# Kernel optimization log

Measured on AMD Instinct MI355X. Metric: run time of the kernel, lower is better.

The kernel has to match this reference:

```python
import jax, jax.numpy as jnp
import numpy as np

B = 256
H, W = 8, 16          # input_resolution for channels=256
C = 768               # dim = channels*3
WS = 4                # window_size
SHIFT = 2             # shift_size
NH = 12               # num_heads
HD = C // NH          # head_dim = 64
HID = 1024            # mlp hidden = channels*4
N = WS * WS           # tokens per window = 16
NW = (H // WS) * (W // WS)  # windows per image = 8
LN_EPS = 1e-5


def _rel_pos_index():
    coords = np.stack(np.meshgrid(np.arange(WS), np.arange(WS), indexing='ij'))  # [2,ws,ws]
    cf = coords.reshape(2, -1)                      # [2, N]
    rel = (cf[:, :, None] - cf[:, None, :]).transpose(1, 2, 0)  # [N, N, 2]
    rel[:, :, 0] += WS - 1
    rel[:, :, 1] += WS - 1
    rel[:, :, 0] *= 2 * WS - 1
    return jnp.asarray(rel.sum(-1))                 # [N, N] int


def _attn_mask():
    img = np.zeros((H, W))
    slices = (slice(0, -WS), slice(-WS, -SHIFT), slice(-SHIFT, None))
    cnt = 0
    for hs in slices:
        for ws_ in slices:
            img[hs, ws_] = cnt
            cnt += 1
    mw = img.reshape(H // WS, WS, W // WS, WS).transpose(0, 2, 1, 3).reshape(-1, N)  # [nW, N]
    am = mw[:, None, :] - mw[:, :, None]            # [nW, N, N]
    return jnp.asarray(np.where(am != 0, -100.0, 0.0).astype(np.float32))


REL_IDX = _rel_pos_index()
ATTN_MASK = _attn_mask()


def _ln(x, g, b):
    m = x.mean(-1, keepdims=True)
    v = ((x - m) ** 2).mean(-1, keepdims=True)
    return (x - m) / jnp.sqrt(v + LN_EPS) * g + b


def setup_inputs() -> dict:
    key = jax.random.key(0)
    ks = jax.random.split(key, 8)
    s = 0.02
    return {
        'x': jax.random.normal(ks[0], (B, H * W, C), jnp.float32),
        'ln1_g': jnp.ones((C,), jnp.float32),
        'ln1_b': jnp.zeros((C,), jnp.float32),
        'qkv_w': jax.random.normal(ks[1], (C, 3 * C), jnp.float32) * s,
        'qkv_b': jnp.zeros((3 * C,), jnp.float32),
        'proj_w': jax.random.normal(ks[2], (C, C), jnp.float32) * s,
        'proj_b': jnp.zeros((C,), jnp.float32),
        'rel_table': jax.random.normal(ks[3], ((2 * WS - 1) * (2 * WS - 1), NH), jnp.float32) * s,
        'ln2_g': jnp.ones((C,), jnp.float32),
        'ln2_b': jnp.zeros((C,), jnp.float32),
        'fc1_w': jax.random.normal(ks[4], (C, HID), jnp.float32) * s,
        'fc1_b': jax.random.normal(ks[5], (HID,), jnp.float32) * 1e-6,
        'fc2_w': jax.random.normal(ks[6], (HID, C), jnp.float32) * s,
        'fc2_b': jax.random.normal(ks[7], (C,), jnp.float32) * 1e-6,
    }


def reference(x, ln1_g, ln1_b, qkv_w, qkv_b, proj_w, proj_b, rel_table,
              ln2_g, ln2_b, fc1_w, fc1_b, fc2_w, fc2_b):
    # --- norm1 + cyclic shift + window partition ---
    h = _ln(x, ln1_g, ln1_b).reshape(B, H, W, C)
    h = jnp.roll(h, (-SHIFT, -SHIFT), axis=(1, 2))
    hw = h.reshape(B, H // WS, WS, W // WS, WS, C).transpose(0, 1, 3, 2, 4, 5)
    hw = hw.reshape(B * NW, N, C)                   # (num_windows*B, N, C)
    # --- window attention with relative position bias + shift mask ---
    qkv = (hw @ qkv_w + qkv_b).reshape(B * NW, N, 3, NH, HD).transpose(2, 0, 3, 1, 4)
    q, k, v = qkv[0] * (HD ** -0.5), qkv[1], qkv[2]  # [Bn, NH, N, HD]
    attn = jnp.einsum('bhnd,bhmd->bhnm', q, k)      # [Bn, NH, N, N]
    bias = rel_table[REL_IDX].transpose(2, 0, 1)    # [NH, N, N]
    attn = attn + bias[None]
    attn = attn.reshape(B, NW, NH, N, N) + ATTN_MASK[None, :, None]
    attn = jax.nn.softmax(attn.reshape(B * NW, NH, N, N), axis=-1)
    o = jnp.einsum('bhnm,bhmd->bhnd', attn, v).transpose(0, 2, 1, 3).reshape(B * NW, N, C)
    o = o @ proj_w + proj_b
    # --- window reverse + reverse shift + residual ---
    o = o.reshape(B, H // WS, W // WS, WS, WS, C).transpose(0, 1, 3, 2, 4, 5).reshape(B, H, W, C)
    o = jnp.roll(o, (SHIFT, SHIFT), axis=(1, 2)).reshape(B, H * W, C)
    x = x + o
    # --- MLP block (dropout is identity at inference) ---
    y = _ln(x, ln2_g, ln2_b)
    y = jax.nn.gelu(y @ fc1_w + fc1_b, approximate=False)
    return x + (y @ fc2_w + fc2_b)
```

## Files before the change

### kernel.cpp

```cpp
#include <hip/hip_runtime.h>
#include <stdint.h>
#include <stddef.h>

typedef __attribute__((ext_vector_type(8))) short bf16x8;
typedef __attribute__((ext_vector_type(4))) float f32x4;
typedef __attribute__((ext_vector_type(4))) unsigned int uint4v;

static __device__ __forceinline__ unsigned short f2bf(float f) {
  unsigned int u = __builtin_bit_cast(unsigned int, f);
  unsigned int r = (u + 0x7FFFu + ((u >> 16) & 1u)) >> 16;
  return (unsigned short)r;
}
static __device__ __forceinline__ float bf2f(unsigned short h) {
  unsigned int u = ((unsigned int)h) << 16;
  return __builtin_bit_cast(float, u);
}
static __device__ __forceinline__ unsigned int pk2(float a, float b) {
  return (unsigned int)f2bf(a) | ((unsigned int)f2bf(b) << 16);
}

static __device__ __forceinline__ void gld16(const void* g, void* l) {
  __builtin_amdgcn_global_load_lds(
      (const __attribute__((address_space(1))) void*)g,
      (__attribute__((address_space(3))) void*)l, 16, 0, 0);
}

__global__ void transpose_cast_all(const float* __restrict__ s0, unsigned short* __restrict__ d0,
                                   const float* __restrict__ s1, unsigned short* __restrict__ d1,
                                   const float* __restrict__ s2, unsigned short* __restrict__ d2,
                                   const float* __restrict__ s3, unsigned short* __restrict__ d3) {
  __shared__ float tile[32][33];
  const int b = blockIdx.x;
  const float* src; unsigned short* dst; int R, C, nbx, bi;
  if (b < 1728)      { src = s0; dst = d0; R = 768;  C = 2304; nbx = 72; bi = b; }
  else if (b < 2304) { src = s1; dst = d1; R = 768;  C = 768;  nbx = 24; bi = b - 1728; }
  else if (b < 3072) { src = s2; dst = d2; R = 768;  C = 1024; nbx = 32; bi = b - 2304; }
  else               { src = s3; dst = d3; R = 1024; C = 768;  nbx = 24; bi = b - 3072; }
  const int bx = bi % nbx, by = bi / nbx;
  const int c0 = bx * 32, r0 = by * 32;
  const int tx = threadIdx.x, ty = threadIdx.y;
  #pragma unroll
  for (int i = 0; i < 32; i += 8)
    tile[ty + i][tx] = src[(size_t)(r0 + ty + i) * C + c0 + tx];
  __syncthreads();
  #pragma unroll
  for (int i = 0; i < 32; i += 8)
    dst[(size_t)(c0 + ty + i) * R + r0 + tx] = f2bf(tile[tx][ty + i]);
}

static __device__ __forceinline__ float blksum256(float v, float* sb) {
  #pragma unroll
  for (int o = 32; o > 0; o >>= 1) v += __shfl_down(v, o, 64);
  int lane = threadIdx.x & 63, w = threadIdx.x >> 6;
  __syncthreads();
  if (lane == 0) sb[w] = v;
  __syncthreads();
  return sb[0] + sb[1] + sb[2] + sb[3];
}

template <int MODE>
__global__ __launch_bounds__(256) void ln_kernel(const float* __restrict__ xf,
                                                 const unsigned short* __restrict__ xb,
                                                 const float* __restrict__ gg,
                                                 const float* __restrict__ bb,
                                                 unsigned short* __restrict__ out) {
  __shared__ float sb[4];
  const int d = blockIdx.x;
  size_t srow;
  if (MODE == 0) {
    int b = d >> 7, wid = (d >> 4) & 7, tok = d & 15;
    int oh = (((wid >> 2) << 2) + (tok >> 2) + 2) & 7;
    int ow = (((wid & 3) << 2) + (tok & 3) + 2) & 15;
    srow = (size_t)(b << 7) + oh * 16 + ow;
  } else {
    srow = d;
  }
  const int t = threadIdx.x;
  const bool ex = t < 128;
  float a0, a1, b0 = 0.f, b1 = 0.f;
  if (MODE == 0) {
    const float2* f2 = (const float2*)(xf + srow * 768);
    float2 p = f2[t]; a0 = p.x; a1 = p.y;
    if (ex) { float2 q = f2[256 + t]; b0 = q.x; b1 = q.y; }
  } else {
    const unsigned int* u = (const unsigned int*)(xb + srow * 768);
    unsigned int p = u[t];
    a0 = bf2f((unsigned short)p); a1 = bf2f((unsigned short)(p >> 16));
    if (ex) {
      unsigned int q = u[256 + t];
      b0 = bf2f((unsigned short)q); b1 = bf2f((unsigned short)(q >> 16));
    }
  }
  float mean = blksum256(a0 + a1 + b0 + b1, sb) * (1.0f / 768.0f);
  float da0 = a0 - mean, da1 = a1 - mean, db0 = b0 - mean, db1 = b1 - mean;
  float var = blksum256(da0 * da0 + da1 * da1 + (ex ? db0 * db0 + db1 * db1 : 0.f), sb) *
              (1.0f / 768.0f);
  float rstd = rsqrtf(var + 1e-5f);
  const float2* g2 = (const float2*)gg;
  const float2* be2 = (const float2*)bb;
  unsigned int* o32 = (unsigned int*)(out + (size_t)d * 768);
  float2 g = g2[t], be = be2[t];
  o32[t] = pk2(da0 * rstd * g.x + be.x, da1 * rstd * g.y + be.y);
  if (ex) {
    float2 gq = g2[256 + t], bq = be2[256 + t];
    o32[256 + t] = pk2(db0 * rstd * gq.x + bq.x, db1 * rstd * gq.y + bq.y);
  }
}

template <int EPI>
__global__ __launch_bounds__(512, 2) void gemm256(
    const unsigned short* __restrict__ A, const unsigned short* __restrict__ BT,
    const float* __restrict__ bias, float* __restrict__ outF,
    unsigned short* __restrict__ outB, const float* __restrict__ resid,
    const unsigned short* __restrict__ residB,
    int M, int N, int K, int NT) {
  __shared__ __align__(16) unsigned short sA[2][256 * 64];
  __shared__ __align__(16) unsigned short sB[2][256 * 64];

  const int tid = threadIdx.x;
  const int lane = tid & 63, wv = tid >> 6;
  const int wr = wv >> 2, wc = wv & 3;
  const int fr = lane & 15, q4 = (lane >> 4) << 2;

  const int nwg = gridDim.x;
  const int orig = blockIdx.x;
  const int swz = (orig & 7) * (nwg >> 3) + (orig >> 3);
  const int mt = swz / NT, nt = swz - mt * NT;
  const int m0 = mt << 8, n0 = nt << 8;

  const size_t K2 = (size_t)K * 2;

  const int srow = tid >> 3;
  const int sg = tid & 7;
  const int sgs = ((sg ^ (srow & 7)) << 4);
  const char* pA = (const char*)A + (size_t)(m0 + srow) * K2 + sgs;
  const char* pB = (const char*)BT + (size_t)(n0 + srow) * K2 + sgs;
  char* sdA = (char*)&sA[0][0] + (wv << 10);
  char* sdB = (char*)&sB[0][0] + (wv << 10);

  const int g0 = (((lane >> 4) ^ (fr & 7)) << 4);
  const int g1 = (((4 + (lane >> 4)) ^ (fr & 7)) << 4);
  const int arow = (wr << 7) + fr;
  const int brow = (wc << 6) + fr;

  f32x4 acc[8][4];
  #pragma unroll
  for (int i = 0; i < 8; ++i)
    #pragma unroll
    for (int j = 0; j < 4; ++j) acc[i][j] = (f32x4){0.f, 0.f, 0.f, 0.f};

  bf16x8 af[4][2];
  bf16x8 bbv[2][2][2];
  const int KT = K >> 6;
  const int NI = KT >> 1;

#define BARR __builtin_amdgcn_s_barrier()
#define LGKM0 asm volatile("s_waitcnt lgkmcnt(0)" ::: "memory")
#define VM6 asm volatile("s_waitcnt vmcnt(6)" ::: "memory")
#define VM0 asm volatile("s_waitcnt vmcnt(0)" ::: "memory")

#define LDA(CB, mh)                                                          \
  {                                                                          \
    const char* ba = ((const char*)&sA[0][0]) + (CB)*32768;                  \
    _Pragma("unroll") for (int fm = 0; fm < 4; ++fm) {                       \
      const int r = arow + (mh)*64 + fm * 16;                                \
      af[fm][0] = *(const bf16x8*)(ba + r * 128 + g0);                       \
      af[fm][1] = *(const bf16x8*)(ba + r * 128 + g1);                       \
    }                                                                        \
  }
#define LDB(CB, nh)                                                          \
  {                                                                          \
    const char* ba = ((const char*)&sB[0][0]) + (CB)*32768;                  \
    _Pragma("unroll") for (int fn = 0; fn < 2; ++fn) {                       \
      const int r = brow + (nh)*32 + fn * 16;                                \
      bbv[nh][fn][0] = *(const bf16x8*)(ba + r * 128 + g0);                  \
      bbv[nh][fn][1] = *(const bf16x8*)(ba + r * 128 + g1);                  \
    }                                                                        \
  }
#define STGA(CB, tt, j)                                                      \
  gld16(pA + (size_t)((j)*64) * K2 + ((size_t)(tt) << 7),                    \
        sdA + (CB)*32768 + (j)*8192);
#define STGB(CB, tt, j)                                                      \
  gld16(pB + (size_t)((j)*64) * K2 + ((size_t)(tt) << 7),                    \
        sdB + (CB)*32768 + (j)*8192);
#define MMAQ(mh, nh)                                                         \
  _Pragma("unroll") for (int fm = 0; fm < 4; ++fm)                           \
      _Pragma("unroll") for (int fn = 0; fn < 2; ++fn) {                     \
    f32x4* ac = &acc[(mh)*4 + fm][(nh)*2 + fn];                              \
    *ac = __builtin_amdgcn_mfma_f32_16x16x32_bf16(af[fm][0], bbv[nh][fn][0], \
                                                  *ac, 0, 0, 0);             \
    *ac = __builtin_amdgcn_mfma_f32_16x16x32_bf16(af[fm][1], bbv[nh][fn][1], \
                                                  *ac, 0, 0, 0);             \
  }
#define OPEN  BARR; LGKM0; __builtin_amdgcn_s_setprio(1)
#define CLOSE __builtin_amdgcn_s_setprio(0)

  #pragma unroll
  for (int j = 0; j < 4; ++j) { STGA(0, 0, j); STGB(0, 0, j); }
  STGA(1, 1, 0); STGA(1, 1, 2);
  STGB(1, 1, 0); STGB(1, 1, 1); STGB(1, 1, 2); STGB(1, 1, 3);
  VM6;
  BARR;

  for (int i = 0; i < NI; ++i) {
    const int s1 = 2 * i + 1, s2 = 2 * i + 2, s3 = 2 * i + 3;
    const bool gl = (i + 1 < NI);
    LDB(0, 0) LDA(0, 0)
    STGA(1, s1, 1); STGA(1, s1, 3);
    OPEN; MMAQ(0, 0); CLOSE; BARR;
    LDB(0, 1)
    if (gl) { STGA(0, s2, 0); STGA(0, s2, 2); }
    OPEN; MMAQ(0, 1); CLOSE; BARR;
    LDA(0, 1)
    if (gl) { STGB(0, s2, 0); STGB(0, s2, 1); }
    OPEN; MMAQ(1, 1); CLOSE; BARR;
    if (gl) { STGB(0, s2, 2); STGB(0, s2, 3); }
    OPEN; MMAQ(1, 0); CLOSE;
    if (gl) { VM6; } else { VM0; }
    BARR;
    LDB(1, 0) LDA(1, 0)
    if (gl) { STGA(0, s2, 1); STGA(0, s2, 3); }
    OPEN; MMAQ(0, 0); CLOSE; BARR;
    LDB(1, 1)
    if (gl) { STGA(1, s3, 0); STGA(1, s3, 2); }
    OPEN; MMAQ(0, 1); CLOSE; BARR;
    LDA(1, 1)
    if (gl) { STGB(1, s3, 0); STGB(1, s3, 1); }
    OPEN; MMAQ(1, 1); CLOSE; BARR;
    if (gl) { STGB(1, s3, 2); STGB(1, s3, 3); }
    OPEN; MMAQ(1, 0); CLOSE;
    if (gl) { VM6; }
    BARR;
  }
#undef BARR
#undef LGKM0
#undef VM6
#undef VM0
#undef LDA
#undef LDB
#undef STGA
#undef STGB
#undef MMAQ
#undef OPEN
#undef CLOSE

  #pragma unroll
  for (int ai = 0; ai < 8; ++ai) {
    #pragma unroll
    for (int bj = 0; bj < 4; ++bj) {
      const int col = n0 + (wc << 6) + bj * 16 + fr;
      const float bc = bias[col];
      #pragma unroll
      for (int i = 0; i < 4; ++i) {
        const int row = m0 + (wr << 7) + ai * 16 + q4 + i;
        float v = acc[ai][bj][i] + bc;
        if (EPI == 0) {
          outB[(size_t)row * N + col] = f2bf(v);
        } else if (EPI == 1) {
          int b = row >> 7, wid = (row >> 4) & 7, tok = row & 15;
          int oh = (((wid >> 2) << 2) + (tok >> 2) + 2) & 7;
          int ow = (((wid & 3) << 2) + (tok & 3) + 2) & 15;
          size_t di = ((size_t)(b << 7) + oh * 16 + ow) * 768 + col;
          outB[di] = f2bf(v + resid[di]);
        } else if (EPI == 2) {
          float g = 0.5f * v * (1.0f + erff(v * 0.70710678118f));
          outB[(size_t)row * N + col] = f2bf(g);
        } else {
          size_t di = (size_t)row * N + col;
          outF[di] = v + bf2f(residB[di]);
        }
      }
    }
  }
}

__global__ __launch_bounds__(64) void attn_win(const unsigned short* __restrict__ qkv,
                                               const float* __restrict__ rel_table,
                                               unsigned short* __restrict__ o) {
  __shared__ __align__(16) unsigned short vt_s[64 * 32];
  __shared__ __align__(16) unsigned short p_s[16 * 32];
  __shared__ __align__(16) unsigned short o_s[16 * 72];
  const int nwg = gridDim.x;
  const int orig = blockIdx.x;
  const int bid = (orig & 7) * (nwg >> 3) + (orig >> 3);
  const int win = bid / 12;
  const int head = bid - win * 12;
  const int wid = win & 7;
  const int lane = threadIdx.x;
  const unsigned short* qb = qkv + (size_t)win * 16 * 2304 + head * 64;
  const int t = lane >> 2, d0 = (lane & 3) << 4;
  unsigned short vv[16];
  *(uint4v*)&vv[0] = *(const uint4v*)(qb + 1536 + (size_t)t * 2304 + d0);
  *(uint4v*)&vv[8] = *(const uint4v*)(qb + 1544 + (size_t)t * 2304 + d0);
  #pragma unroll
  for (int e = 0; e < 16; ++e) vt_s[(d0 + e) * 32 + t] = vv[e];
  #pragma unroll
  for (int e = 0; e < 16; ++e) vt_s[lane * 32 + 16 + e] = 0;
  if (lane < 16) {
    #pragma unroll
    for (int e = 0; e < 16; ++e) p_s[lane * 32 + 16 + e] = 0;
  }
  __syncthreads();

  const int fr = lane & 15, g8 = (lane >> 4) << 3;
  const unsigned short* qrow = qb + (size_t)fr * 2304;
  bf16x8 qa0 = *(const bf16x8*)(qrow + g8);
  bf16x8 qa1 = *(const bf16x8*)(qrow + 32 + g8);
  bf16x8 ka0 = *(const bf16x8*)(qrow + 768 + g8);
  bf16x8 ka1 = *(const bf16x8*)(qrow + 800 + g8);
  f32x4 s = (f32x4){0.f, 0.f, 0.f, 0.f};
  s = __builtin_amdgcn_mfma_f32_16x16x32_bf16(qa0, ka0, s, 0, 0, 0);
  s = __builtin_amdgcn_mfma_f32_16x16x32_bf16(qa1, ka1, s, 0, 0, 0);

  const int wh = wid >> 2, wwc = wid & 3;
  const int rj = fr >> 2, cj = fr & 3;
  const int rowm = wh * 4 + rj, colm = wwc * 4 + cj;
  const int rgm = (rowm < 4 ? 0 : (rowm < 6 ? 1 : 2)) * 3 +
                  (colm < 12 ? 0 : (colm < 14 ? 1 : 2));
  float p[4];
  #pragma unroll
  for (int i = 0; i < 4; ++i) {
    int n = ((lane >> 4) << 2) + i;
    int ri = n >> 2, ci = n & 3;
    int rown = wh * 4 + ri, coln = wwc * 4 + ci;
    int rgn = (rown < 4 ? 0 : (rown < 6 ? 1 : 2)) * 3 +
              (coln < 12 ? 0 : (coln < 14 ? 1 : 2));
    float bias = rel_table[(size_t)((ri - rj + 3) * 7 + (ci - cj + 3)) * 12 + head];
    p[i] = s[i] * 0.125f + bias + (rgn != rgm ? -100.0f : 0.0f);
  }
  float mx[4] = {p[0], p[1], p[2], p[3]};
  #pragma unroll
  for (int off = 8; off > 0; off >>= 1)
    #pragma unroll
    for (int i = 0; i < 4; ++i) mx[i] = fmaxf(mx[i], __shfl_xor(mx[i], off, 64));
  float sm[4];
  #pragma unroll
  for (int i = 0; i < 4; ++i) { p[i] = __expf(p[i] - mx[i]); sm[i] = p[i]; }
  #pragma unroll
  for (int off = 8; off > 0; off >>= 1)
    #pragma unroll
    for (int i = 0; i < 4; ++i) sm[i] += __shfl_xor(sm[i], off, 64);
  #pragma unroll
  for (int i = 0; i < 4; ++i)
    p_s[(((lane >> 4) << 2) + i) * 32 + fr] = f2bf(p[i] / sm[i]);
  __syncthreads();

  bf16x8 pa = *(const bf16x8*)&p_s[fr * 32 + g8];
  const f32x4 oz = (f32x4){0.f, 0.f, 0.f, 0.f};
  #pragma unroll
  for (int c = 0; c < 4; ++c) {
    bf16x8 vb = *(const bf16x8*)&vt_s[(c * 16 + fr) * 32 + g8];
    f32x4 oa = __builtin_amdgcn_mfma_f32_16x16x32_bf16(pa, vb, oz, 0, 0, 0);
    #pragma unroll
    for (int i = 0; i < 4; ++i) {
      int n = ((lane >> 4) << 2) + i;
      o_s[n * 72 + c * 16 + fr] = f2bf(oa[i]);
    }
  }
  __syncthreads();
  const int orow = lane >> 2, oq = lane & 3;
  const unsigned short* srcp = &o_s[orow * 72 + oq * 16];
  unsigned short* dstp = o + ((size_t)win * 16 + orow) * 768 + head * 64 + oq * 16;
  *(uint4v*)dstp = *(const uint4v*)srcp;
  *(uint4v*)(dstp + 8) = *(const uint4v*)(srcp + 8);
}

extern "C" void kernel_launch(void* const* d_in, const int* in_sizes, int n_in,
                              void* d_out, int out_size, void* d_ws, size_t ws_size,
                              hipStream_t stream) {
  const float* x      = (const float*)d_in[0];
  const float* ln1_g  = (const float*)d_in[1];
  const float* ln1_b  = (const float*)d_in[2];
  const float* qkv_w  = (const float*)d_in[3];
  const float* qkv_b  = (const float*)d_in[4];
  const float* proj_w = (const float*)d_in[5];
  const float* proj_b = (const float*)d_in[6];
  const float* rel_t  = (const float*)d_in[7];
  const float* ln2_g  = (const float*)d_in[8];
  const float* ln2_b  = (const float*)d_in[9];
  const float* fc1_w  = (const float*)d_in[10];
  const float* fc1_b  = (const float*)d_in[11];
  const float* fc2_w  = (const float*)d_in[12];
  const float* fc2_b  = (const float*)d_in[13];
  float* out = (float*)d_out;

  char* ws = (char*)d_ws;
  unsigned short* wsA = (unsigned short*)(ws);
  unsigned short* qkvb = (unsigned short*)(ws + 50331648);
  unsigned short* xr16 = (unsigned short*)(ws + 50331648);
  unsigned short* h1 = (unsigned short*)(ws + 201326592);
  unsigned short* qkv_wT = (unsigned short*)(ws + 268435456);
  unsigned short* proj_wT = (unsigned short*)(ws + 271974400);
  unsigned short* fc1_wT = (unsigned short*)(ws + 273154048);
  unsigned short* fc2_wT = (unsigned short*)(ws + 274726912);

  transpose_cast_all<<<3840, dim3(32, 8), 0, stream>>>(qkv_w, qkv_wT, proj_w, proj_wT,
                                                       fc1_w, fc1_wT, fc2_w, fc2_wT);

  ln_kernel<0><<<32768, 256, 0, stream>>>(x, nullptr, ln1_g, ln1_b, wsA);
  gemm256<0><<<dim3(128 * 9), 512, 0, stream>>>(wsA, qkv_wT, qkv_b, nullptr, qkvb,
                                                nullptr, nullptr,
                                                32768, 2304, 768, 9);
  attn_win<<<24576, 64, 0, stream>>>(qkvb, rel_t, wsA);
  gemm256<1><<<dim3(128 * 3), 512, 0, stream>>>(wsA, proj_wT, proj_b, nullptr, xr16,
                                                x, nullptr,
                                                32768, 768, 768, 3);
  ln_kernel<2><<<32768, 256, 0, stream>>>(nullptr, xr16, ln2_g, ln2_b, wsA);
  gemm256<2><<<dim3(128 * 4), 512, 0, stream>>>(wsA, fc1_wT, fc1_b, nullptr, h1,
                                                nullptr, nullptr,
                                                32768, 1024, 768, 4);
  gemm256<3><<<dim3(128 * 3), 512, 0, stream>>>(h1, fc2_wT, fc2_b, out, nullptr,
                                                nullptr, xr16,
                                                32768, 768, 1024, 3);
}
```

Baseline: 511.4 us.

## Make GEMM kernels persistent and prefetch next tile during last K iteration

Converts the four GEMM launches into persistent kernels with 256 workgroups that loop over output tiles with a stride of 256. In the final K iteration each workgroup starts loading the first K slices of its next tile into the double buffers, hiding that tile's startup latency behind the current epilogue. This trades the hardware scheduler's dynamic load balance for a static assignment, which can leave tail imbalance. With 256 workgroups and launch bounds of 2 per CU, only about one workgroup runs per CU, so occupancy may drop.

```diff
diff --git a/kernel.cpp b/kernel.cpp
--- a/kernel.cpp
+++ b/kernel.cpp
@@ -113,7 +113,7 @@
     const float* __restrict__ bias, float* __restrict__ outF,
     unsigned short* __restrict__ outB, const float* __restrict__ resid,
     const unsigned short* __restrict__ residB,
-    int M, int N, int K, int NT) {
+    int M, int N, int K, int NT, int NTILES) {
   __shared__ __align__(16) unsigned short sA[2][256 * 64];
   __shared__ __align__(16) unsigned short sB[2][256 * 64];
 
@@ -122,19 +122,10 @@
   const int wr = wv >> 2, wc = wv & 3;
   const int fr = lane & 15, q4 = (lane >> 4) << 2;
 
-  const int nwg = gridDim.x;
-  const int orig = blockIdx.x;
-  const int swz = (orig & 7) * (nwg >> 3) + (orig >> 3);
-  const int mt = swz / NT, nt = swz - mt * NT;
-  const int m0 = mt << 8, n0 = nt << 8;
-
   const size_t K2 = (size_t)K * 2;
-
   const int srow = tid >> 3;
   const int sg = tid & 7;
   const int sgs = ((sg ^ (srow & 7)) << 4);
-  const char* pA = (const char*)A + (size_t)(m0 + srow) * K2 + sgs;
-  const char* pB = (const char*)BT + (size_t)(n0 + srow) * K2 + sgs;
   char* sdA = (char*)&sA[0][0] + (wv << 10);
   char* sdB = (char*)&sB[0][0] + (wv << 10);
 
@@ -142,6 +133,23 @@
   const int g1 = (((4 + (lane >> 4)) ^ (fr & 7)) << 4);
   const int arow = (wr << 7) + fr;
   const int brow = (wc << 6) + fr;
+
+  int v = blockIdx.x;
+  if (v >= NTILES) return;
+  int sw = (v & 7) * (NTILES >> 3) + (v >> 3);
+  int m0 = (sw / NT) << 8, n0 = (sw - (sw / NT) * NT) << 8;
+  const char* pA = (const char*)A + (size_t)(m0 + srow) * K2 + sgs;
+  const char* pB = (const char*)BT + (size_t)(n0 + srow) * K2 + sgs;
+  int vn = v + 256;
+  bool more = vn < NTILES;
+  int m0n = m0, n0n = n0;
+  const char* pAn = pA; const char* pBn = pB;
+  if (more) {
+    int sw2 = (vn & 7) * (NTILES >> 3) + (vn >> 3);
+    m0n = (sw2 / NT) << 8; n0n = (sw2 - (sw2 / NT) * NT) << 8;
+    pAn = (const char*)A + (size_t)(m0n + srow) * K2 + sgs;
+    pBn = (const char*)BT + (size_t)(n0n + srow) * K2 + sgs;
+  }
 
   f32x4 acc[8][4];
   #pragma unroll
@@ -177,11 +185,11 @@
       bbv[nh][fn][1] = *(const bf16x8*)(ba + r * 128 + g1);                  \
     }                                                                        \
   }
-#define STGA(CB, tt, j)                                                      \
-  gld16(pA + (size_t)((j)*64) * K2 + ((size_t)(tt) << 7),                    \
+#define STGA_(P, CB, tt, j)                                                  \
+  gld16((P) + (size_t)((j)*64) * K2 + ((size_t)(tt) << 7),                   \
         sdA + (CB)*32768 + (j)*8192);
-#define STGB(CB, tt, j)                                                      \
-  gld16(pB + (size_t)((j)*64) * K2 + ((size_t)(tt) << 7),                    \
+#define STGB_(P, CB, tt, j)                                                  \
+  gld16((P) + (size_t)((j)*64) * K2 + ((size_t)(tt) << 7),                   \
         sdB + (CB)*32768 + (j)*8192);
 #define MMAQ(mh, nh)                                                         \
   _Pragma("unroll") for (int fm = 0; fm < 4; ++fm)                           \
@@ -196,41 +204,90 @@
 #define CLOSE __builtin_amdgcn_s_setprio(0)
 
   #pragma unroll
-  for (int j = 0; j < 4; ++j) { STGA(0, 0, j); STGB(0, 0, j); }
-  STGA(1, 1, 0); STGA(1, 1, 2);
-  STGB(1, 1, 0); STGB(1, 1, 1); STGB(1, 1, 2); STGB(1, 1, 3);
+  for (int j = 0; j < 4; ++j) { STGA_(pA, 0, 0, j); STGB_(pB, 0, 0, j); }
+  STGA_(pA, 1, 1, 0); STGA_(pA, 1, 1, 2);
+  STGB_(pB, 1, 1, 0); STGB_(pB, 1, 1, 1); STGB_(pB, 1, 1, 2); STGB_(pB, 1, 1, 3);
   VM6;
   BARR;
 
-  for (int i = 0; i < NI; ++i) {
-    const int s1 = 2 * i + 1, s2 = 2 * i + 2, s3 = 2 * i + 3;
-    const bool gl = (i + 1 < NI);
-    LDB(0, 0) LDA(0, 0)
-    STGA(1, s1, 1); STGA(1, s1, 3);
-    OPEN; MMAQ(0, 0); CLOSE; BARR;
-    LDB(0, 1)
-    if (gl) { STGA(0, s2, 0); STGA(0, s2, 2); }
-    OPEN; MMAQ(0, 1); CLOSE; BARR;
-    LDA(0, 1)
-    if (gl) { STGB(0, s2, 0); STGB(0, s2, 1); }
-    OPEN; MMAQ(1, 1); CLOSE; BARR;
-    if (gl) { STGB(0, s2, 2); STGB(0, s2, 3); }
-    OPEN; MMAQ(1, 0); CLOSE;
-    if (gl) { VM6; } else { VM0; }
-    BARR;
-    LDB(1, 0) LDA(1, 0)
-    if (gl) { STGA(0, s2, 1); STGA(0, s2, 3); }
-    OPEN; MMAQ(0, 0); CLOSE; BARR;
-    LDB(1, 1)
-    if (gl) { STGA(1, s3, 0); STGA(1, s3, 2); }
-    OPEN; MMAQ(0, 1); CLOSE; BARR;
-    LDA(1, 1)
-    if (gl) { STGB(1, s3, 0); STGB(1, s3, 1); }
-    OPEN; MMAQ(1, 1); CLOSE; BARR;
-    if (gl) { STGB(1, s3, 2); STGB(1, s3, 3); }
-    OPEN; MMAQ(1, 0); CLOSE;
-    if (gl) { VM6; }
-    BARR;
+  for (;;) {
+    for (int i = 0; i < NI; ++i) {
+      const bool lastit = (i == NI - 1);
+      const int s1 = 2 * i + 1;
+      const bool gl = (!lastit) || more;
+      const char* qA = lastit ? pAn : pA;
+      const char* qB = lastit ? pBn : pB;
+      const int t2 = lastit ? 0 : 2 * i + 2;
+      const int t3 = lastit ? 1 : 2 * i + 3;
+      LDB(0, 0) LDA(0, 0)
+      STGA_(pA, 1, s1, 1); STGA_(pA, 1, s1, 3);
+      OPEN; MMAQ(0, 0); CLOSE; BARR;
+      LDB(0, 1)
+      if (gl) { STGA_(qA, 0, t2, 0); STGA_(qA, 0, t2, 2); }
+      OPEN; MMAQ(0, 1); CLOSE; BARR;
+      LDA(0, 1)
+      if (gl) { STGB_(qB, 0, t2, 0); STGB_(qB, 0, t2, 1); }
+      OPEN; MMAQ(1, 1); CLOSE; BARR;
+      if (gl) { STGB_(qB, 0, t2, 2); STGB_(qB, 0, t2, 3); }
+      OPEN; MMAQ(1, 0); CLOSE;
+      if (gl) { VM6; } else { VM0; }
+      BARR;
+      LDB(1, 0) LDA(1, 0)
+      if (gl) { STGA_(qA, 0, t2, 1); STGA_(qA, 0, t2, 3); }
+      OPEN; MMAQ(0, 0); CLOSE; BARR;
+      LDB(1, 1)
+      if (gl) { STGA_(qA, 1, t3, 0); STGA_(qA, 1, t3, 2); }
+      OPEN; MMAQ(0, 1); CLOSE; BARR;
+      LDA(1, 1)
+      if (gl) { STGB_(qB, 1, t3, 0); STGB_(qB, 1, t3, 1); }
+      OPEN; MMAQ(1, 1); CLOSE; BARR;
+      if (gl) { STGB_(qB, 1, t3, 2); STGB_(qB, 1, t3, 3); }
+      OPEN; MMAQ(1, 0); CLOSE;
+      if (gl) { VM6; }
+      BARR;
+    }
+
+    #pragma unroll
+    for (int ai = 0; ai < 8; ++ai) {
+      #pragma unroll
+      for (int bj = 0; bj < 4; ++bj) {
+        const int col = n0 + (wc << 6) + bj * 16 + fr;
+        const float bc = bias[col];
+        #pragma unroll
+        for (int i = 0; i < 4; ++i) {
+          const int row = m0 + (wr << 7) + ai * 16 + q4 + i;
+          float vvv = acc[ai][bj][i] + bc;
+          if (EPI == 0) {
+            outB[(size_t)row * N + col] = f2bf(vvv);
+          } else if (EPI == 1) {
+            int b = row >> 7, wid = (row >> 4) & 7, tok = row & 15;
+            int oh = (((wid >> 2) << 2) + (tok >> 2) + 2) & 7;
+            int ow = (((wid & 3) << 2) + (tok & 3) + 2) & 15;
+            size_t di = ((size_t)(b << 7) + oh * 16 + ow) * 768 + col;
+            outB[di] = f2bf(vvv + resid[di]);
+          } else if (EPI == 2) {
+            float g = 0.5f * vvv * (1.0f + erff(vvv * 0.70710678118f));
+            outB[(size_t)row * N + col] = f2bf(g);
+          } else {
+            size_t di = (size_t)row * N + col;
+            outF[di] = vvv + bf2f(residB[di]);
+          }
+          acc[ai][bj][i] = 0.f;
+        }
+      }
+    }
+
+    v = vn;
+    if (v >= NTILES) break;
+    pA = pAn; pB = pBn; m0 = m0n; n0 = n0n;
+    vn += 256;
+    more = (vn < NTILES);
+    if (more) {
+      int sw2 = (vn & 7) * (NTILES >> 3) + (vn >> 3);
+      m0n = (sw2 / NT) << 8; n0n = (sw2 - (sw2 / NT) * NT) << 8;
+      pAn = (const char*)A + (size_t)(m0n + srow) * K2 + sgs;
+      pBn = (const char*)BT + (size_t)(n0n + srow) * K2 + sgs;
+    }
   }
 #undef BARR
 #undef LGKM0
@@ -238,40 +295,11 @@
 #undef VM0
 #undef LDA
 #undef LDB
-#undef STGA
-#undef STGB
+#undef STGA_
+#undef STGB_
 #undef MMAQ
 #undef OPEN
 #undef CLOSE
-
-  #pragma unroll
-  for (int ai = 0; ai < 8; ++ai) {
-    #pragma unroll
-    for (int bj = 0; bj < 4; ++bj) {
-      const int col = n0 + (wc << 6) + bj * 16 + fr;
-      const float bc = bias[col];
-      #pragma unroll
-      for (int i = 0; i < 4; ++i) {
-        const int row = m0 + (wr << 7) + ai * 16 + q4 + i;
-        float v = acc[ai][bj][i] + bc;
-        if (EPI == 0) {
-          outB[(size_t)row * N + col] = f2bf(v);
-        } else if (EPI == 1) {
-          int b = row >> 7, wid = (row >> 4) & 7, tok = row & 15;
-          int oh = (((wid >> 2) << 2) + (tok >> 2) + 2) & 7;
-          int ow = (((wid & 3) << 2) + (tok & 3) + 2) & 15;
-          size_t di = ((size_t)(b << 7) + oh * 16 + ow) * 768 + col;
-          outB[di] = f2bf(v + resid[di]);
-        } else if (EPI == 2) {
-          float g = 0.5f * v * (1.0f + erff(v * 0.70710678118f));
-          outB[(size_t)row * N + col] = f2bf(g);
-        } else {
-          size_t di = (size_t)row * N + col;
-          outF[di] = v + bf2f(residB[di]);
-        }
-      }
-    }
-  }
 }
 
 __global__ __launch_bounds__(64) void attn_win(const unsigned short* __restrict__ qkv,
@@ -398,18 +426,18 @@
                                                        fc1_w, fc1_wT, fc2_w, fc2_wT);
 
   ln_kernel<0><<<32768, 256, 0, stream>>>(x, nullptr, ln1_g, ln1_b, wsA);
-  gemm256<0><<<dim3(128 * 9), 512, 0, stream>>>(wsA, qkv_wT, qkv_b, nullptr, qkvb,
-                                                nullptr, nullptr,
-                                                32768, 2304, 768, 9);
+  gemm256<0><<<256, 512, 0, stream>>>(wsA, qkv_wT, qkv_b, nullptr, qkvb,
+                                      nullptr, nullptr,
+                                      32768, 2304, 768, 9, 1152);
   attn_win<<<24576, 64, 0, stream>>>(qkvb, rel_t, wsA);
-  gemm256<1><<<dim3(128 * 3), 512, 0, stream>>>(wsA, proj_wT, proj_b, nullptr, xr16,
-                                                x, nullptr,
-                                                32768, 768, 768, 3);
+  gemm256<1><<<256, 512, 0, stream>>>(wsA, proj_wT, proj_b, nullptr, xr16,
+                                      x, nullptr,
+                                      32768, 768, 768, 3, 384);
   ln_kernel<2><<<32768, 256, 0, stream>>>(nullptr, xr16, ln2_g, ln2_b, wsA);
-  gemm256<2><<<dim3(128 * 4), 512, 0, stream>>>(wsA, fc1_wT, fc1_b, nullptr, h1,
-                                                nullptr, nullptr,
-                                                32768, 1024, 768, 4);
-  gemm256<3><<<dim3(128 * 3), 512, 0, stream>>>(h1, fc2_wT, fc2_b, out, nullptr,
-                                                nullptr, xr16,
-                                                32768, 768, 1024, 3);
-}
+  gemm256<2><<<256, 512, 0, stream>>>(wsA, fc1_wT, fc1_b, nullptr, h1,
+                                      nullptr, nullptr,
+                                      32768, 1024, 768, 4, 512);
+  gemm256<3><<<256, 512, 0, stream>>>(h1, fc2_wT, fc2_b, out, nullptr,
+                                      nullptr, xr16,
+                                      32768, 768, 1024, 3, 384);
+}
```

Measured after the change: 498.6 us. 2.5% less time.
